# Kernel tuning notes

Hardware: AMD Instinct MI355X
Metric: run time of the kernel (lower is better)

## Reference

```python
import jax, jax.numpy as jnp
import numpy as np
import math

V, D, H, NL, L, B = 32000, 1024, 16, 6, 1024, 2
HD = D // H
EPS = 1e-5


def _positional(L, D):
    # matches torch: exp(arange(0,D,2) * -(log(1000)/D))
    div = jnp.exp(jnp.arange(0, D, 2, dtype=jnp.float32) * (-math.log(1000.0) / D))
    k = jnp.arange(L, dtype=jnp.float32)[:, None]
    pos = jnp.zeros((L, D), dtype=jnp.float32)
    pos = pos.at[:, 0::2].set(jnp.sin(k * div))
    pos = pos.at[:, 1::2].set(jnp.cos(k * div))
    return pos[None]  # [1, L, D]


def setup_inputs() -> dict:
    key = jax.random.key(0)
    ks = jax.random.split(key, 12)
    s = 0.02
    tokens = jax.random.randint(ks[0], (B, L), 0, V)
    emb = jax.random.normal(ks[1], (V, D), jnp.float32) * s
    pos = _positional(L, D)
    ln1_g = jnp.ones((NL, D), jnp.float32)
    ln1_b = jnp.zeros((NL, D), jnp.float32)
    ln2_g = jnp.ones((NL, D), jnp.float32)
    ln2_b = jnp.zeros((NL, D), jnp.float32)
    attn_w = jax.random.normal(ks[2], (NL, D, 3 * D), jnp.float32) * s
    attn_b = jnp.zeros((NL, 3 * D), jnp.float32)
    proj_w = jax.random.normal(ks[3], (NL, D, D), jnp.float32) * s
    proj_b = jnp.zeros((NL, D), jnp.float32)
    mlp_w1 = jax.random.normal(ks[4], (NL, D, 4 * D), jnp.float32) * s
    mlp_b1 = jnp.zeros((NL, 4 * D), jnp.float32)
    mlp_w2 = jax.random.normal(ks[5], (NL, 4 * D, D), jnp.float32) * s
    mlp_b2 = jnp.zeros((NL, D), jnp.float32)
    out_w = jax.random.normal(ks[6], (D, V), jnp.float32) * s
    return dict(tokens=tokens, pos=pos, emb=emb,
                ln1_g=ln1_g, ln1_b=ln1_b, ln2_g=ln2_g, ln2_b=ln2_b,
                attn_w=attn_w, attn_b=attn_b, proj_w=proj_w, proj_b=proj_b,
                mlp_w1=mlp_w1, mlp_b1=mlp_b1, mlp_w2=mlp_w2, mlp_b2=mlp_b2,
                out_w=out_w)


def _ln(x, g, b):
    mu = jnp.mean(x, -1, keepdims=True)
    var = jnp.mean(jnp.square(x - mu), -1, keepdims=True)
    return (x - mu) * jax.lax.rsqrt(var + EPS) * g + b


def _block(x, p, causal_mask):
    ln1_g, ln1_b, ln2_g, ln2_b, aw, ab, pw, pb, w1, b1, w2, b2 = p
    h = _ln(x, ln1_g, ln1_b)
    qkv = h @ aw + ab                      # [B, L, 3D]
    q, k, v = jnp.split(qkv, 3, axis=-1)
    Bc, Lc = x.shape[0], x.shape[1]
    q = q.reshape(Bc, Lc, H, HD)
    k = k.reshape(Bc, Lc, H, HD)
    v = v.reshape(Bc, Lc, H, HD)
    scores = jnp.einsum('blhd,bmhd->bhlm', q, k) * (1.0 / math.sqrt(HD))
    scores = jnp.where(causal_mask, scores, -jnp.inf)
    attn = jax.nn.softmax(scores, axis=-1)
    y = jnp.einsum('bhlm,bmhd->blhd', attn, v).reshape(Bc, Lc, D)
    x = x + (y @ pw + pb)
    r = _ln(x, ln2_g, ln2_b)
    # NOTE: original ModuleList order applies GELU AFTER the second linear
    r = jax.nn.gelu((r @ w1 + b1) @ w2 + b2, approximate=False)
    return x + r


def reference(tokens, pos, emb, ln1_g, ln1_b, ln2_g, ln2_b,
              attn_w, attn_b, proj_w, proj_b,
              mlp_w1, mlp_b1, mlp_w2, mlp_b2, out_w):
    x = emb[tokens] + pos                  # [B, L, D]
    Lc = x.shape[1]
    causal_mask = jnp.tril(jnp.ones((Lc, Lc), bool))[None, None]
    for i in range(NL):
        p = (ln1_g[i], ln1_b[i], ln2_g[i], ln2_b[i],
             attn_w[i], attn_b[i], proj_w[i], proj_b[i],
             mlp_w1[i], mlp_b1[i], mlp_w2[i], mlp_b2[i])
        x = _block(x, p, causal_mask)
    return x @ out_w                       # [B, L, V] logits
```

## Files before the change

### kernel.cpp

```cpp
#include <hip/hip_runtime.h>
#include <hip/hip_bf16.h>
#include <math.h>

typedef __bf16 bf16;
typedef __bf16 bf16x4 __attribute__((ext_vector_type(4)));
typedef __bf16 bf16x8 __attribute__((ext_vector_type(8)));
typedef float f32x4 __attribute__((ext_vector_type(4)));

__device__ __forceinline__ void gld_lds16(const void* g, void* l) {
    __builtin_amdgcn_global_load_lds(
        (const __attribute__((address_space(1))) unsigned int*)g,
        (__attribute__((address_space(3))) unsigned int*)l, 16, 0, 0);
}

#define VMW(n) asm volatile("s_waitcnt vmcnt(" #n ")" ::: "memory")
#define BARR() asm volatile("s_barrier" ::: "memory")

__global__ __launch_bounds__(256) void k_embed(const int* __restrict__ tok,
                                               const float* __restrict__ emb,
                                               const float* __restrict__ pos,
                                               float* __restrict__ x) {
    int row = blockIdx.x;
    int l = row & 1023;
    int tk = tok[row];
    const float4* e = (const float4*)(emb + (size_t)tk * 1024);
    const float4* p = (const float4*)(pos + (size_t)l * 1024);
    float4* o = (float4*)(x + (size_t)row * 1024);
    float4 a = e[threadIdx.x], b = p[threadIdx.x];
    o[threadIdx.x] = make_float4(a.x + b.x, a.y + b.y, a.z + b.z, a.w + b.w);
}

__global__ __launch_bounds__(256) void k_ln(const float* __restrict__ x,
                                            const float* __restrict__ g,
                                            const float* __restrict__ b,
                                            bf16* __restrict__ out) {
    int row = blockIdx.x;
    int t = threadIdx.x;
    const float4* xr = (const float4*)(x + (size_t)row * 1024);
    float4 v = xr[t];
    float s1 = v.x + v.y + v.z + v.w;
    float s2 = v.x * v.x + v.y * v.y + v.z * v.z + v.w * v.w;
#pragma unroll
    for (int o = 32; o; o >>= 1) { s1 += __shfl_down(s1, o); s2 += __shfl_down(s2, o); }
    __shared__ float ps1[4], ps2[4], stat[2];
    int lane = t & 63, wid = t >> 6;
    if (lane == 0) { ps1[wid] = s1; ps2[wid] = s2; }
    __syncthreads();
    if (t == 0) {
        float a1 = ps1[0] + ps1[1] + ps1[2] + ps1[3];
        float a2 = ps2[0] + ps2[1] + ps2[2] + ps2[3];
        float mu = a1 * (1.f / 1024.f);
        float var = a2 * (1.f / 1024.f) - mu * mu;
        stat[0] = mu; stat[1] = rsqrtf(var + 1e-5f);
    }
    __syncthreads();
    float mu = stat[0], rs = stat[1];
    const float4* gv = (const float4*)g;
    const float4* bv = (const float4*)b;
    float4 gg = gv[t], bb = bv[t];
    bf16x4 o4;
    o4[0] = (bf16)((v.x - mu) * rs * gg.x + bb.x);
    o4[1] = (bf16)((v.y - mu) * rs * gg.y + bb.y);
    o4[2] = (bf16)((v.z - mu) * rs * gg.z + bb.z);
    o4[3] = (bf16)((v.w - mu) * rs * gg.w + bb.w);
    *(bf16x4*)(out + (size_t)row * 1024 + t * 4) = o4;
}

__device__ __forceinline__ void transpose64(const float* __restrict__ W,
                                            bf16* __restrict__ WT,
                                            int K, int N, int n0, int k0, int t,
                                            float (*tile)[65]) {
    int tx = t & 15, ty = t >> 4;
#pragma unroll
    for (int i = 0; i < 64; i += 16) {
        float4 v = *(const float4*)&W[(size_t)(k0 + ty + i) * N + n0 + tx * 4];
        tile[ty + i][tx * 4 + 0] = v.x;
        tile[ty + i][tx * 4 + 1] = v.y;
        tile[ty + i][tx * 4 + 2] = v.z;
        tile[ty + i][tx * 4 + 3] = v.w;
    }
    __syncthreads();
    int n = t >> 3, ks = t & 7;
#pragma unroll
    for (int pass = 0; pass < 2; ++pass) {
        int nn = n + pass * 32;
        bf16x8 v;
#pragma unroll
        for (int j = 0; j < 8; ++j) v[j] = (bf16)tile[ks * 8 + j][nn];
        *(bf16x8*)&WT[(size_t)(n0 + nn) * K + k0 + ks * 8] = v;
    }
}

__device__ __forceinline__ void tr_layer_block(int bid,
                                               const float* aw, const float* pw,
                                               const float* m1, const float* m2,
                                               bf16* wT, int t, float (*tile)[65]) {
    const float* src; bf16* dst; int K, N, tn, tk;
    if (bid < 768)       { src = aw; dst = wT;            K = 1024; N = 3072; tn = bid % 48; tk = bid / 48; }
    else if (bid < 1024) { int b = bid - 768;  src = pw; dst = wT + 3145728; K = 1024; N = 1024; tn = b % 16; tk = b / 16; }
    else if (bid < 2048) { int b = bid - 1024; src = m1; dst = wT + 4194304; K = 1024; N = 4096; tn = b % 64; tk = b / 64; }
    else                 { int b = bid - 2048; src = m2; dst = wT + 8388608; K = 4096; N = 1024; tn = b % 16; tk = b / 16; }
    transpose64(src, dst, K, N, tn * 64, tk * 64, t, tile);
}

__global__ __launch_bounds__(256) void k_transpose_layer(const float* __restrict__ aw,
                                                         const float* __restrict__ pw,
                                                         const float* __restrict__ m1,
                                                         const float* __restrict__ m2,
                                                         bf16* __restrict__ wT) {
    __shared__ float tile[64][65];
    tr_layer_block(blockIdx.x, aw, pw, m1, m2, wT, threadIdx.x, tile);
}

__device__ __forceinline__ void stage128(const char* Ab, const char* Bb,
                                         char* As, char* Bs, int Kb, int k0b, int t) {
#pragma unroll
    for (int j = 0; j < 4; ++j) {
        int idx = j * 256 + t;
        int row = idx >> 3;
        int cb = (idx & 7) << 4;
        int scb = cb ^ ((row & 7) << 4);
        gld_lds16(Ab + (size_t)row * Kb + k0b + scb, As + idx * 16);
        gld_lds16(Bb + (size_t)row * Kb + k0b + scb, Bs + idx * 16);
    }
}

template <int EPI>
__global__ __launch_bounds__(256) void k_gemm2(const bf16* __restrict__ A,
                                               const bf16* __restrict__ BT,
                                               const float* __restrict__ bias,
                                               const float* __restrict__ resid,
                                               float* __restrict__ outf,
                                               bf16* __restrict__ outb,
                                               int N, int K) {
    __shared__ __align__(16) bf16 As[2][128 * 64];
    __shared__ __align__(16) bf16 Bs[2][128 * 64];
    int per = gridDim.x >> 3;
    int tile = (blockIdx.x & 7) * per + (blockIdx.x >> 3);
    int bm = tile & 15, bn = tile >> 4;
    int t = threadIdx.x, lane = t & 63;
    int wr = t >> 7, wc = (t >> 6) & 1;
    f32x4 acc[4][4] = {};
    const char* Ab = (const char*)(A + (size_t)bm * 128 * K);
    const char* Bb = (const char*)(BT + (size_t)bn * 128 * K);
    int Kb = K * 2;
    int nk = K >> 6;
    stage128(Ab, Bb, (char*)As[0], (char*)Bs[0], Kb, 0, t);
    VMW(0); BARR();
    for (int tt = 0; tt < nk; ++tt) {
        int cur = tt & 1;
        if (tt + 1 < nk)
            stage128(Ab, Bb, (char*)As[cur ^ 1], (char*)Bs[cur ^ 1], Kb, (tt + 1) * 128, t);
        const char* Ac = (const char*)As[cur];
        const char* Bc = (const char*)Bs[cur];
#pragma unroll
        for (int kk = 0; kk < 2; ++kk) {
            bf16x8 af[4], bfr[4];
            int cb = kk * 64 + ((lane >> 4) << 4);
#pragma unroll
            for (int m = 0; m < 4; ++m) {
                int r = wr * 64 + m * 16 + (lane & 15);
                af[m] = *(const bf16x8*)(Ac + r * 128 + (cb ^ ((r & 7) << 4)));
            }
#pragma unroll
            for (int n = 0; n < 4; ++n) {
                int r = wc * 64 + n * 16 + (lane & 15);
                bfr[n] = *(const bf16x8*)(Bc + r * 128 + (cb ^ ((r & 7) << 4)));
            }
#pragma unroll
            for (int m = 0; m < 4; ++m)
#pragma unroll
                for (int n = 0; n < 4; ++n)
                    acc[m][n] = __builtin_amdgcn_mfma_f32_16x16x32_bf16(af[m], bfr[n], acc[m][n], 0, 0, 0);
        }
        VMW(0); BARR();
    }
    int row0 = bm * 128 + wr * 64 + ((lane >> 4) << 2);
    int col0 = bn * 128 + wc * 64 + (lane & 15);
#pragma unroll
    for (int m = 0; m < 4; ++m) {
#pragma unroll
        for (int n = 0; n < 4; ++n) {
            int col = col0 + n * 16;
            float bv = bias[col];
#pragma unroll
            for (int r = 0; r < 4; ++r) {
                int row = row0 + m * 16 + r;
                size_t idx = (size_t)row * N + col;
                float v = acc[m][n][r] + bv;
                if (EPI == 0) {
                    outb[idx] = (bf16)v;
                } else if (EPI == 1) {
                    outf[idx] = resid[idx] + v;
                } else {
                    outf[idx] = resid[idx] + 0.5f * v * (1.0f + erff(v * 0.70710678118f));
                }
            }
        }
    }
}

__device__ __forceinline__ void stage64(const char* Ab, const char* Bb,
                                        char* As, char* Bs, int Kb, int k0b, int t) {
#pragma unroll
    for (int j = 0; j < 2; ++j) {
        int idx = j * 256 + t;
        int row = idx >> 3;
        int cb = (idx & 7) << 4;
        int scb = cb ^ ((row & 7) << 4);
        gld_lds16(Ab + (size_t)row * Kb + k0b + scb, As + idx * 16);
        gld_lds16(Bb + (size_t)row * Kb + k0b + scb, Bs + idx * 16);
    }
}

template <int EPI>
__global__ __launch_bounds__(256) void k_gemm64(const bf16* __restrict__ A,
                                                const bf16* __restrict__ BT,
                                                const float* __restrict__ bias,
                                                const float* __restrict__ resid,
                                                float* __restrict__ outf,
                                                bf16* __restrict__ outb,
                                                int N, int K) {
    __shared__ __align__(16) bf16 As[2][64 * 64];
    __shared__ __align__(16) bf16 Bs[2][64 * 64];
    int per = gridDim.x >> 3;
    int tile = (blockIdx.x & 7) * per + (blockIdx.x >> 3);
    int bm = tile & 31, bn = tile >> 5;
    int t = threadIdx.x, lane = t & 63, wid = t >> 6;
    f32x4 acc[4] = {};
    const char* Ab = (const char*)(A + (size_t)bm * 64 * K);
    const char* Bb = (const char*)(BT + (size_t)bn * 64 * K);
    int Kb = K * 2;
    int nk = K >> 6;
    stage64(Ab, Bb, (char*)As[0], (char*)Bs[0], Kb, 0, t);
    VMW(0); BARR();
    for (int tt = 0; tt < nk; ++tt) {
        int cur = tt & 1;
        if (tt + 1 < nk)
            stage64(Ab, Bb, (char*)As[cur ^ 1], (char*)Bs[cur ^ 1], Kb, (tt + 1) * 128, t);
        const char* Ac = (const char*)As[cur];
        const char* Bc = (const char*)Bs[cur];
#pragma unroll
        for (int kk = 0; kk < 2; ++kk) {
            int cb = kk * 64 + ((lane >> 4) << 4);
            int ra = wid * 16 + (lane & 15);
            bf16x8 af = *(const bf16x8*)(Ac + ra * 128 + (cb ^ ((ra & 7) << 4)));
            bf16x8 bfr[4];
#pragma unroll
            for (int n = 0; n < 4; ++n) {
                int r = n * 16 + (lane & 15);
                bfr[n] = *(const bf16x8*)(Bc + r * 128 + (cb ^ ((r & 7) << 4)));
            }
#pragma unroll
            for (int n = 0; n < 4; ++n)
                acc[n] = __builtin_amdgcn_mfma_f32_16x16x32_bf16(af, bfr[n], acc[n], 0, 0, 0);
        }
        VMW(0); BARR();
    }
    int row0 = bm * 64 + wid * 16 + ((lane >> 4) << 2);
    int col0 = bn * 64 + (lane & 15);
#pragma unroll
    for (int n = 0; n < 4; ++n) {
        int col = col0 + n * 16;
        float bv = bias[col];
#pragma unroll
        for (int r = 0; r < 4; ++r) {
            int row = row0 + r;
            size_t idx = (size_t)row * N + col;
            float v = acc[n][r] + bv;
            float res;
            if (EPI == 1) {
                res = resid[idx] + v;
            } else {
                res = resid[idx] + 0.5f * v * (1.0f + erff(v * 0.70710678118f));
            }
            outf[idx] = res;
            if (outb) outb[idx] = (bf16)res;
        }
    }
}

__device__ __forceinline__ void stage_full256(const char* gtile, char* ldst,
                                              int Kb, int t) {
#pragma unroll
    for (int j = 0; j < 4; ++j) {
        int idx = j * 512 + t;
        int row = idx >> 3;
        int cb = (idx & 7) << 4;
        int scb = cb ^ ((row & 7) << 4);
        gld_lds16(gtile + (size_t)row * Kb + scb, ldst + idx * 16);
    }
}

__device__ __forceinline__ void stage_half256(const char* gtile, char* ldst,
                                              int Kb, int t, int half) {
#pragma unroll
    for (int j = 0; j < 2; ++j) {
        int idx = (half * 2 + j) * 512 + t;
        int row = idx >> 3;
        int cb = (idx & 7) << 4;
        int scb = cb ^ ((row & 7) << 4);
        gld_lds16(gtile + (size_t)row * Kb + scb, ldst + idx * 16);
    }
}

template <int MH, int NH>
__device__ __forceinline__ void phase_rd(const char* Ac, const char* Bc,
                                         int lrow, int lk, int wm, int wn,
                                         bf16x8 (&af)[4][2], bf16x8 (&bfr)[2][2]) {
#pragma unroll
    for (int kk = 0; kk < 2; ++kk) {
        int cb = kk * 64 + lk * 16;
#pragma unroll
        for (int m = 0; m < 4; ++m) {
            int row = (MH * 4 + m) * 32 + wm * 16 + lrow;
            af[m][kk] = *(const bf16x8*)(Ac + row * 128 + (cb ^ ((row & 7) << 4)));
        }
#pragma unroll
        for (int n = 0; n < 2; ++n) {
            int row = (NH * 2 + n) * 64 + wn * 16 + lrow;
            bfr[n][kk] = *(const bf16x8*)(Bc + row * 128 + (cb ^ ((row & 7) << 4)));
        }
    }
}

template <int MH, int NH>
__device__ __forceinline__ void phase_mm(bf16x8 (&af)[4][2], bf16x8 (&bfr)[2][2],
                                         f32x4 (&acc)[8][4]) {
    __builtin_amdgcn_s_setprio(1);
#pragma unroll
    for (int kk = 0; kk < 2; ++kk)
#pragma unroll
        for (int m = 0; m < 4; ++m)
#pragma unroll
            for (int n = 0; n < 2; ++n)
                acc[MH * 4 + m][NH * 2 + n] = __builtin_amdgcn_mfma_f32_16x16x32_bf16(
                    af[m][kk], bfr[n][kk], acc[MH * 4 + m][NH * 2 + n], 0, 0, 0);
    __builtin_amdgcn_s_setprio(0);
    __builtin_amdgcn_sched_barrier(0);
}

__global__ __launch_bounds__(512, 1) void k_gemm256(const bf16* __restrict__ A,
                                                    const bf16* __restrict__ BT,
                                                    float* __restrict__ outf,
                                                    int N, int K) {
    __shared__ __align__(16) bf16 Asb[2][256 * 64];
    __shared__ __align__(16) bf16 Bsb[3][256 * 64];
    int t = threadIdx.x, lane = t & 63, wid = t >> 6;
    int wm = wid >> 2, wn = wid & 3;
    int lrow = lane & 15, lk = lane >> 4;
    int tile = (blockIdx.x & 7) * 125 + (blockIdx.x >> 3);
    int bm = tile & 7;
    int bn = tile >> 3;

    const char* Ab = (const char*)(A + (size_t)bm * 256 * K);
    const char* Bb = (const char*)(BT + (size_t)bn * 256 * K);
    int Kb = K * 2;
    int nk = K >> 6;
    f32x4 acc[8][4] = {};

    stage_full256(Ab, (char*)Asb[0], Kb, t);
    stage_full256(Bb, (char*)Bsb[0], Kb, t);
    stage_full256(Bb + 128, (char*)Bsb[1], Kb, t);

    for (int tt = 0; tt < nk; ++tt) {
        int ka = (tt + 1 < nk) ? tt + 1 : nk - 1;
        int kb = (tt + 2 < nk) ? tt + 2 : nk - 1;
        const char* Ac = (const char*)Asb[tt & 1];
        const char* Bc = (const char*)Bsb[tt % 3];
        char* An = (char*)Asb[(tt + 1) & 1];
        char* Bn = (char*)Bsb[(tt + 2) % 3];
        const char* Ag = Ab + (size_t)ka * 128;
        const char* Bg = Bb + (size_t)kb * 128;
        VMW(4); BARR();
        bf16x8 af[4][2], bfr[2][2];
        phase_rd<0, 0>(Ac, Bc, lrow, lk, wm, wn, af, bfr);
        stage_half256(Ag, An, Kb, t, 0);
        BARR();
        phase_mm<0, 0>(af, bfr, acc);
        BARR();
        phase_rd<0, 1>(Ac, Bc, lrow, lk, wm, wn, af, bfr);
        stage_half256(Ag, An, Kb, t, 1);
        BARR();
        phase_mm<0, 1>(af, bfr, acc);
        BARR();
        phase_rd<1, 0>(Ac, Bc, lrow, lk, wm, wn, af, bfr);
        stage_half256(Bg, Bn, Kb, t, 0);
        BARR();
        phase_mm<1, 0>(af, bfr, acc);
        BARR();
        phase_rd<1, 1>(Ac, Bc, lrow, lk, wm, wn, af, bfr);
        stage_half256(Bg, Bn, Kb, t, 1);
        BARR();
        phase_mm<1, 1>(af, bfr, acc);
        BARR();
    }

    size_t row0 = (size_t)bm * 256 + wm * 16 + (lane >> 4) * 4;
    int col0 = bn * 256 + wn * 16 + (lane & 15);
#pragma unroll
    for (int mi = 0; mi < 8; ++mi) {
#pragma unroll
        for (int ni = 0; ni < 4; ++ni) {
            int col = col0 + ni * 64;
#pragma unroll
            for (int r = 0; r < 4; ++r) {
                size_t row = row0 + mi * 32 + r;
                outf[row * N + col] = acc[mi][ni][r];
            }
        }
    }
}

__global__ __launch_bounds__(256) void k_attn_tr(const bf16* __restrict__ qkv,
                                                 bf16* __restrict__ y,
                                                 const float* __restrict__ aw,
                                                 const float* __restrict__ pw,
                                                 const float* __restrict__ m1,
                                                 const float* __restrict__ m2,
                                                 bf16* __restrict__ wTnext,
                                                 const float* __restrict__ outw,
                                                 bf16* __restrict__ outT) {
    __shared__ __align__(16) char smem[49152];
    int bidg = blockIdx.x;
    int t = threadIdx.x;
    if (bidg >= 256) {
        int tb = bidg - 256;
        float (*tile)[65] = (float(*)[65])smem;
        if (aw) {
            tr_layer_block(tb, aw, pw, m1, m2, wTnext, t, tile);
        } else {
            int tn = tb % 500, tk = tb / 500;
            transpose64(outw, outT, 1024, 32000, tn * 64, tk * 64, t, tile);
        }
        return;
    }
    bf16* Qs  = (bf16*)smem;
    bf16* KsA = Qs + 4096;
    bf16* KsB = KsA + 4096;
    bf16* VtA = KsB + 4096;
    bf16* VtB = VtA + 4096;
    bf16* Ps  = VtB + 4096;
    int tile = (bidg & 7) * 32 + (bidg >> 3);
    int qbp = tile & 7;
    int bh = tile >> 3;
    int b = bh >> 4, h = bh & 15;
    int lane = t & 63, wid = t >> 6;
    int lr = lane & 15, lk = lane >> 4;
    int tok0 = b << 10;
    const char* qbase = (const char*)qkv;
    int kvr = t >> 2, d0v = (t & 3) * 16;

    auto stageK = [&](int kv0, bf16* Kb) {
#pragma unroll
        for (int j = 0; j < 2; ++j) {
            int off = (j * 256 + t) * 16;
            int row = off >> 7, colb = off & 127;
            int scb = colb ^ ((row & 7) << 4);
            gld_lds16(qbase + ((size_t)(tok0 + kv0 + row) * 3072 + 1024 + h * 64) * 2 + scb,
                      (char*)Kb + off);
        }
    };
    bf16x4 vreg[4];
    auto loadV = [&](int kv0) {
        const bf16* vrow = qkv + (size_t)(tok0 + kv0 + kvr) * 3072 + 2048 + h * 64 + d0v;
#pragma unroll
        for (int e4 = 0; e4 < 4; ++e4) vreg[e4] = *(const bf16x4*)(vrow + e4 * 4);
    };
    auto writeV = [&](bf16* Vb) {
#pragma unroll
        for (int e4 = 0; e4 < 4; ++e4)
#pragma unroll
            for (int i2 = 0; i2 < 4; ++i2) {
                int d = d0v + e4 * 4 + i2;
                Vb[d * 64 + (kvr ^ ((d & 7) << 3))] = vreg[e4][i2];
            }
    };

    for (int ph = 0; ph < 2; ++ph) {
        int qb = ph ? (15 - qbp) : qbp;
        int q0 = qb << 6;
#pragma unroll
        for (int j = 0; j < 2; ++j) {
            int off = (j * 256 + t) * 16;
            int row = off >> 7, colb = off & 127;
            int scb = colb ^ ((row & 7) << 4);
            gld_lds16(qbase + ((size_t)(tok0 + q0 + row) * 3072 + h * 64) * 2 + scb,
                      (char*)Qs + off);
        }
        stageK(0, KsA);
        loadV(0);
        VMW(0);
        writeV(VtA);
        __syncthreads();

        int qrw = wid * 16 + lr;
        int qsw = (qrw & 7) << 4;
        bf16x8 aq0 = *(const bf16x8*)((const char*)Qs + qrw * 128 + ((lk * 16) ^ qsw));
        bf16x8 aq1 = *(const bf16x8*)((const char*)Qs + qrw * 128 + ((64 + lk * 16) ^ qsw));
        f32x4 o[4] = {};
        float mrun[4], lrun[4];
#pragma unroll
        for (int r = 0; r < 4; ++r) { mrun[r] = -INFINITY; lrun[r] = 0.f; }
        int qrow = q0 + wid * 16 + lk * 4;
        int nt = qb + 1;

        for (int ti = 0; ti < nt; ++ti) {
            int kv0 = ti << 6;
            bf16* Kc = (ti & 1) ? KsB : KsA;
            bf16* Vc = (ti & 1) ? VtB : VtA;
            bf16* Kn = (ti & 1) ? KsA : KsB;
            bf16* Vn = (ti & 1) ? VtA : VtB;
            bool pf = (ti + 1 < nt);
            if (pf) { stageK((ti + 1) << 6, Kn); loadV((ti + 1) << 6); }
            f32x4 s[4];
#pragma unroll
            for (int n = 0; n < 4; ++n) {
                int krw = n * 16 + lr;
                int ksw = (krw & 7) << 4;
                const char* kb = (const char*)Kc + krw * 128;
                bf16x8 bk0 = *(const bf16x8*)(kb + ((lk * 16) ^ ksw));
                bf16x8 bk1 = *(const bf16x8*)(kb + ((64 + lk * 16) ^ ksw));
                f32x4 z = {};
                z = __builtin_amdgcn_mfma_f32_16x16x32_bf16(aq0, bk0, z, 0, 0, 0);
                z = __builtin_amdgcn_mfma_f32_16x16x32_bf16(aq1, bk1, z, 0, 0, 0);
                s[n] = z;
            }
            float mx[4];
#pragma unroll
            for (int r = 0; r < 4; ++r) mx[r] = -INFINITY;
#pragma unroll
            for (int n = 0; n < 4; ++n) {
                int col = kv0 + n * 16 + lr;
#pragma unroll
                for (int r = 0; r < 4; ++r) {
                    float sv = s[n][r] * 0.125f;
                    sv = (col <= qrow + r) ? sv : -INFINITY;
                    s[n][r] = sv;
                    mx[r] = fmaxf(mx[r], sv);
                }
            }
#pragma unroll
            for (int r = 0; r < 4; ++r)
#pragma unroll
                for (int m = 1; m < 16; m <<= 1) mx[r] = fmaxf(mx[r], __shfl_xor(mx[r], m));
            float scl[4];
#pragma unroll
            for (int r = 0; r < 4; ++r) {
                float mn = fmaxf(mrun[r], mx[r]);
                scl[r] = __expf(mrun[r] - mn);
                mrun[r] = mn;
            }
            float rs[4] = {0.f, 0.f, 0.f, 0.f};
#pragma unroll
            for (int n = 0; n < 4; ++n)
#pragma unroll
                for (int r = 0; r < 4; ++r) {
                    float p = __expf(s[n][r] - mrun[r]);
                    s[n][r] = p;
                    rs[r] += p;
                }
#pragma unroll
            for (int r = 0; r < 4; ++r) {
#pragma unroll
                for (int m = 1; m < 16; m <<= 1) rs[r] += __shfl_xor(rs[r], m);
                lrun[r] = lrun[r] * scl[r] + rs[r];
            }
#pragma unroll
            for (int n = 0; n < 4; ++n)
#pragma unroll
                for (int r = 0; r < 4; ++r) {
                    o[n][r] *= scl[r];
                    int prow = lk * 4 + r;
                    Ps[wid * 1024 + prow * 64 + ((n * 16 + lr) ^ ((prow & 7) << 3))] = (bf16)s[n][r];
                }
            int psw = (lr & 7) << 3;
            const bf16* pb = Ps + wid * 1024 + lr * 64;
            bf16x8 ap0 = *(const bf16x8*)(pb + ((lk * 8) ^ psw));
            bf16x8 ap1 = *(const bf16x8*)(pb + ((32 + lk * 8) ^ psw));
#pragma unroll
            for (int n = 0; n < 4; ++n) {
                int vrw = n * 16 + lr;
                int vsw = (vrw & 7) << 3;
                const bf16* vb = Vc + vrw * 64;
                bf16x8 bv0 = *(const bf16x8*)(vb + ((lk * 8) ^ vsw));
                bf16x8 bv1 = *(const bf16x8*)(vb + ((32 + lk * 8) ^ vsw));
                o[n] = __builtin_amdgcn_mfma_f32_16x16x32_bf16(ap0, bv0, o[n], 0, 0, 0);
                o[n] = __builtin_amdgcn_mfma_f32_16x16x32_bf16(ap1, bv1, o[n], 0, 0, 0);
            }
            if (pf) { VMW(0); writeV(Vn); }
            __syncthreads();
        }
#pragma unroll
        for (int n = 0; n < 4; ++n)
#pragma unroll
            for (int r = 0; r < 4; ++r) {
                int row = tok0 + qrow + r;
                y[(size_t)row * 1024 + h * 64 + n * 16 + lr] = (bf16)(o[n][r] / lrun[r]);
            }
    }
}

extern "C" void kernel_launch(void* const* d_in, const int* in_sizes, int n_in,
                              void* d_out, int out_size, void* d_ws, size_t ws_size,
                              hipStream_t stream) {
    const int*   tokens = (const int*)d_in[0];
    const float* pos    = (const float*)d_in[1];
    const float* emb    = (const float*)d_in[2];
    const float* ln1_g  = (const float*)d_in[3];
    const float* ln1_b  = (const float*)d_in[4];
    const float* ln2_g  = (const float*)d_in[5];
    const float* ln2_b  = (const float*)d_in[6];
    const float* attn_w = (const float*)d_in[7];
    const float* attn_b = (const float*)d_in[8];
    const float* proj_w = (const float*)d_in[9];
    const float* proj_b = (const float*)d_in[10];
    const float* mlp_w1 = (const float*)d_in[11];
    const float* mlp_b1 = (const float*)d_in[12];
    const float* mlp_w2 = (const float*)d_in[13];
    const float* mlp_b2 = (const float*)d_in[14];
    const float* out_w  = (const float*)d_in[15];
    float* out = (float*)d_out;

    char* ws = (char*)d_ws;
    size_t off = 0;
    auto alloc = [&](size_t bytes) {
        void* p = ws + off;
        off = (off + bytes + 255) & ~(size_t)255;
        return p;
    };
    float* x   = (float*)alloc((size_t)2048 * 1024 * 4);
    bf16* hb   = (bf16*)alloc((size_t)2048 * 1024 * 2);
    bf16* qkvb = (bf16*)alloc((size_t)2048 * 3072 * 2);
    bf16* yb   = (bf16*)alloc((size_t)2048 * 1024 * 2);
    bf16* hidb = (bf16*)alloc((size_t)2048 * 4096 * 2);
    bf16* outT = (bf16*)alloc((size_t)32000 * 1024 * 2);
    bf16* slot1 = (bf16*)alloc((size_t)9437184 * 2);
    bf16* slots[2] = { outT, slot1 };

    k_embed<<<2048, 256, 0, stream>>>(tokens, emb, pos, x);
    k_transpose_layer<<<3072, 256, 0, stream>>>(attn_w, proj_w, mlp_w1, mlp_w2, slots[0]);

    for (int i = 0; i < 6; ++i) {
        bf16* wT = slots[i & 1];
        k_ln<<<2048, 256, 0, stream>>>(x, ln1_g + i * 1024, ln1_b + i * 1024, hb);
        k_gemm2<0><<<384, 256, 0, stream>>>(hb, wT, attn_b + i * 3072,
                                            nullptr, nullptr, qkvb, 3072, 1024);
        if (i < 5) {
            int j = i + 1;
            k_attn_tr<<<3328, 256, 0, stream>>>(qkvb, yb,
                attn_w + (size_t)j * 1024 * 3072, proj_w + (size_t)j * 1024 * 1024,
                mlp_w1 + (size_t)j * 1024 * 4096, mlp_w2 + (size_t)j * 4096 * 1024,
                slots[j & 1], nullptr, nullptr);
        } else {
            k_attn_tr<<<8256, 256, 0, stream>>>(qkvb, yb,
                nullptr, nullptr, nullptr, nullptr, nullptr, out_w, outT);
        }
        k_gemm64<1><<<512, 256, 0, stream>>>(yb, wT + 3145728, proj_b + i * 1024,
                                             x, x, nullptr, 1024, 1024);
        k_ln<<<2048, 256, 0, stream>>>(x, ln2_g + i * 1024, ln2_b + i * 1024, hb);
        k_gemm2<0><<<512, 256, 0, stream>>>(hb, wT + 4194304, mlp_b1 + i * 4096,
                                            nullptr, nullptr, hidb, 4096, 1024);
        k_gemm64<2><<<512, 256, 0, stream>>>(hidb, wT + 8388608, mlp_b2 + i * 1024,
                                             x, x, (i == 5) ? hb : nullptr, 1024, 4096);
    }

    k_gemm256<<<1000, 512, 0, stream>>>(hb, outT, out, 32000, 1024);
}
```

Before: 1.098 ms.

## Fuse embed with first transpose; lazy softmax rescale and setprio in attention

```diff
diff --git a/kernel.cpp b/kernel.cpp
--- a/kernel.cpp
+++ b/kernel.cpp
@@ -15,20 +15,6 @@
 
 #define VMW(n) asm volatile("s_waitcnt vmcnt(" #n ")" ::: "memory")
 #define BARR() asm volatile("s_barrier" ::: "memory")
-
-__global__ __launch_bounds__(256) void k_embed(const int* __restrict__ tok,
-                                               const float* __restrict__ emb,
-                                               const float* __restrict__ pos,
-                                               float* __restrict__ x) {
-    int row = blockIdx.x;
-    int l = row & 1023;
-    int tk = tok[row];
-    const float4* e = (const float4*)(emb + (size_t)tk * 1024);
-    const float4* p = (const float4*)(pos + (size_t)l * 1024);
-    float4* o = (float4*)(x + (size_t)row * 1024);
-    float4 a = e[threadIdx.x], b = p[threadIdx.x];
-    o[threadIdx.x] = make_float4(a.x + b.x, a.y + b.y, a.z + b.z, a.w + b.w);
-}
 
 __global__ __launch_bounds__(256) void k_ln(const float* __restrict__ x,
                                             const float* __restrict__ g,
@@ -103,13 +89,29 @@
     transpose64(src, dst, K, N, tn * 64, tk * 64, t, tile);
 }
 
-__global__ __launch_bounds__(256) void k_transpose_layer(const float* __restrict__ aw,
-                                                         const float* __restrict__ pw,
-                                                         const float* __restrict__ m1,
-                                                         const float* __restrict__ m2,
-                                                         bf16* __restrict__ wT) {
+__global__ __launch_bounds__(256) void k_embed_tr(const int* __restrict__ tok,
+                                                  const float* __restrict__ emb,
+                                                  const float* __restrict__ pos,
+                                                  float* __restrict__ x,
+                                                  const float* __restrict__ aw,
+                                                  const float* __restrict__ pw,
+                                                  const float* __restrict__ m1,
+                                                  const float* __restrict__ m2,
+                                                  bf16* __restrict__ wT) {
     __shared__ float tile[64][65];
-    tr_layer_block(blockIdx.x, aw, pw, m1, m2, wT, threadIdx.x, tile);
+    int bid = blockIdx.x;
+    if (bid < 2048) {
+        int row = bid;
+        int l = row & 1023;
+        int tk = tok[row];
+        const float4* e = (const float4*)(emb + (size_t)tk * 1024);
+        const float4* p = (const float4*)(pos + (size_t)l * 1024);
+        float4* o = (float4*)(x + (size_t)row * 1024);
+        float4 a = e[threadIdx.x], b = p[threadIdx.x];
+        o[threadIdx.x] = make_float4(a.x + b.x, a.y + b.y, a.z + b.z, a.w + b.w);
+        return;
+    }
+    tr_layer_block(bid - 2048, aw, pw, m1, m2, wT, threadIdx.x, tile);
 }
 
 __device__ __forceinline__ void stage128(const char* Ab, const char* Bb,
@@ -514,6 +516,7 @@
             bool pf = (ti + 1 < nt);
             if (pf) { stageK((ti + 1) << 6, Kn); loadV((ti + 1) << 6); }
             f32x4 s[4];
+            __builtin_amdgcn_s_setprio(1);
 #pragma unroll
             for (int n = 0; n < 4; ++n) {
                 int krw = n * 16 + lr;
@@ -526,6 +529,7 @@
                 z = __builtin_amdgcn_mfma_f32_16x16x32_bf16(aq1, bk1, z, 0, 0, 0);
                 s[n] = z;
             }
+            __builtin_amdgcn_s_setprio(0);
             float mx[4];
 #pragma unroll
             for (int r = 0; r < 4; ++r) mx[r] = -INFINITY;
@@ -544,12 +548,19 @@
             for (int r = 0; r < 4; ++r)
 #pragma unroll
                 for (int m = 1; m < 16; m <<= 1) mx[r] = fmaxf(mx[r], __shfl_xor(mx[r], m));
-            float scl[4];
-#pragma unroll
-            for (int r = 0; r < 4; ++r) {
-                float mn = fmaxf(mrun[r], mx[r]);
-                scl[r] = __expf(mrun[r] - mn);
-                mrun[r] = mn;
+            bool need = false;
+#pragma unroll
+            for (int r = 0; r < 4; ++r) need = need || (mx[r] > mrun[r] + 8.f);
+            if (__any(need)) {
+#pragma unroll
+                for (int r = 0; r < 4; ++r) {
+                    float mn = fmaxf(mrun[r], mx[r]);
+                    float scl = __expf(mrun[r] - mn);
+                    mrun[r] = mn;
+                    lrun[r] *= scl;
+#pragma unroll
+                    for (int n = 0; n < 4; ++n) o[n][r] *= scl;
+                }
             }
             float rs[4] = {0.f, 0.f, 0.f, 0.f};
 #pragma unroll
@@ -557,27 +568,21 @@
 #pragma unroll
                 for (int r = 0; r < 4; ++r) {
                     float p = __expf(s[n][r] - mrun[r]);
-                    s[n][r] = p;
                     rs[r] += p;
+                    int prow = lk * 4 + r;
+                    Ps[wid * 1024 + prow * 64 + ((n * 16 + lr) ^ ((prow & 7) << 3))] = (bf16)p;
                 }
 #pragma unroll
             for (int r = 0; r < 4; ++r) {
 #pragma unroll
                 for (int m = 1; m < 16; m <<= 1) rs[r] += __shfl_xor(rs[r], m);
-                lrun[r] = lrun[r] * scl[r] + rs[r];
-            }
-#pragma unroll
-            for (int n = 0; n < 4; ++n)
-#pragma unroll
-                for (int r = 0; r < 4; ++r) {
-                    o[n][r] *= scl[r];
-                    int prow = lk * 4 + r;
-                    Ps[wid * 1024 + prow * 64 + ((n * 16 + lr) ^ ((prow & 7) << 3))] = (bf16)s[n][r];
-                }
+                lrun[r] += rs[r];
+            }
             int psw = (lr & 7) << 3;
             const bf16* pb = Ps + wid * 1024 + lr * 64;
             bf16x8 ap0 = *(const bf16x8*)(pb + ((lk * 8) ^ psw));
             bf16x8 ap1 = *(const bf16x8*)(pb + ((32 + lk * 8) ^ psw));
+            __builtin_amdgcn_s_setprio(1);
 #pragma unroll
             for (int n = 0; n < 4; ++n) {
                 int vrw = n * 16 + lr;
@@ -588,6 +593,7 @@
                 o[n] = __builtin_amdgcn_mfma_f32_16x16x32_bf16(ap0, bv0, o[n], 0, 0, 0);
                 o[n] = __builtin_amdgcn_mfma_f32_16x16x32_bf16(ap1, bv1, o[n], 0, 0, 0);
             }
+            __builtin_amdgcn_s_setprio(0);
             if (pf) { VMW(0); writeV(Vn); }
             __syncthreads();
         }
@@ -638,8 +644,8 @@
     bf16* slot1 = (bf16*)alloc((size_t)9437184 * 2);
     bf16* slots[2] = { outT, slot1 };
 
-    k_embed<<<2048, 256, 0, stream>>>(tokens, emb, pos, x);
-    k_transpose_layer<<<3072, 256, 0, stream>>>(attn_w, proj_w, mlp_w1, mlp_w2, slots[0]);
+    k_embed_tr<<<5120, 256, 0, stream>>>(tokens, emb, pos, x,
+                                         attn_w, proj_w, mlp_w1, mlp_w2, slots[0]);
 
     for (int i = 0; i < 6; ++i) {
         bf16* wT = slots[i & 1];
```

New measurement: 1.106 ms. No clear change (+0.7%).
